# Optimization experiments

Measured on AMD Instinct MI355X. Metric: run time of the kernel, lower is better.

## Reference

```python
import jax, jax.numpy as jnp
import numpy as np

ALPHA_FAST = 0.74
ALPHA_SLOW = 0.95
EPS = 1e-6


def setup_inputs() -> dict:
    key = jax.random.key(0)
    kA, kU = jax.random.split(key)
    A = jax.random.normal(kA, (8, 16, 64, 64, 64), dtype=jnp.float32)      # [B,M,T,H,W]
    U = jax.random.normal(kU, (8, 16, 2, 64, 64, 64), dtype=jnp.float32)   # [B,M,2,T,H,W]
    return {"A": A, "U": U}


def _ema_last(x, alpha):
    # Closed form of the causal EMA recurrence acc_t = a*acc_{t-1} + (1-a)*x_t,
    # evaluated only at the final timestep (the torch module discards all others):
    # acc_{T-1} = (1-a) * sum_t a^{T-1-t} x_t
    T = x.shape[2]
    t = jnp.arange(T)
    w = ((1.0 - alpha) * alpha ** (T - 1 - t)).astype(x.dtype)
    return jnp.einsum('bmthw,t->bmhw', x, w)


def _quad_energy_last(p):
    # p: [B,M,T,H,W]. quad_energy shifts by 2 frames (edge-replicated); at the
    # last frame: pq = 0.5*(p[T-1] - p[T-3])  (T >= 3).
    pq = 0.5 * (p[:, :, -1] - p[:, :, -3])
    return jnp.sqrt(jnp.maximum(p[:, :, -1] ** 2 + pq ** 2, EPS))


def reference(A, U):
    A_last = A[:, :, -1]                         # [B,M,H,W]
    A_fast = _ema_last(A, ALPHA_FAST)
    A_slow = _ema_last(A, ALPHA_SLOW)
    # torch.diff with prepend -> last element is A[T-1] - A[T-2]
    A_deriv = A[:, :, -1] - A[:, :, -2]
    E_re = _quad_energy_last(U[:, :, 0])
    E_im = _quad_energy_last(U[:, :, 1])
    E_temp = jnp.sqrt(jnp.maximum(E_re ** 2 + E_im ** 2, EPS))
    return jnp.concatenate([A_last, A_fast, A_slow, A_deriv, E_temp], axis=1)  # [B,5M,H,W]
```

## Files before the change

### kernel.cpp

```cpp
#include <hip/hip_runtime.h>
#include <math.h>


#define T_DIM 64
#define HW    4096
#define HALF_T 32

typedef __attribute__((ext_vector_type(4))) float f4v;

__device__ __forceinline__ f4v ntload4(const float* p) {
    return __builtin_nontemporal_load((const f4v*)p);
}

__global__ __launch_bounds__(256, 4) void temporal_summarizer_kernel(
        const float* __restrict__ A, const float* __restrict__ U,
        float* __restrict__ out, float pf32, float ps32) {
    constexpr float AF = 0.74f, AS = 0.95f;
    constexpr float OMF = 1.0f - 0.74f, OMS = 1.0f - 0.95f;
    constexpr float EPS = 1e-6f;

    const int blk   = blockIdx.x;
    const int hh    = blk & 1;
    const int split = (blk >> 1) & 3;
    const int bm    = blk >> 3;
    const int m     = bm & 15;
    const int b     = bm >> 4;

    const int pix = split * (HW / 4) + threadIdx.x * 4;

    const float* pA = A + (size_t)bm * (T_DIM * HW) + (size_t)(hh * HALF_T) * HW + pix;

    f4v fast = 0.f, slow = 0.f;
    f4v a62 = 0.f, a63 = 0.f;

    #pragma unroll 16
    for (int t = 0; t < HALF_T; ++t) {
        f4v x = ntload4(pA + (size_t)t * HW);
        fast = AF * fast + OMF * x;
        slow = AS * slow + OMS * x;
        if (hh && t == HALF_T - 2) a62 = x;
        if (hh && t == HALF_T - 1) a63 = x;
    }

    if (!hh) {
        fast *= pf32;
        slow *= ps32;
    }

    float* ofast = out + ((size_t)(b * 80 + 16 + m)) * HW + pix;
    float* oslow = out + ((size_t)(b * 80 + 32 + m)) * HW + pix;
    #pragma unroll
    for (int i = 0; i < 4; ++i) {
        atomicAdd(&ofast[i], fast[i]);
        atomicAdd(&oslow[i], slow[i]);
    }

    if (hh) {
        const float* pU = U + (size_t)bm * (2 * T_DIM * HW) + pix;
        f4v u0l = ntload4(pU + 63 * HW);
        f4v u0m = ntload4(pU + 61 * HW);
        f4v u1l = ntload4(pU + (size_t)T_DIM * HW + 63 * HW);
        f4v u1m = ntload4(pU + (size_t)T_DIM * HW + 61 * HW);

        f4v et;
        #pragma unroll
        for (int i = 0; i < 4; ++i) {
            float pq0 = 0.5f * (u0l[i] - u0m[i]);
            float er  = sqrtf(fmaxf(u0l[i] * u0l[i] + pq0 * pq0, EPS));
            float pq1 = 0.5f * (u1l[i] - u1m[i]);
            float ei  = sqrtf(fmaxf(u1l[i] * u1l[i] + pq1 * pq1, EPS));
            et[i] = sqrtf(fmaxf(er * er + ei * ei, EPS));
        }

        f4v deriv = a63 - a62;

        float* ob = out + ((size_t)(b * 80 + m)) * HW + pix;
        *(f4v*)(ob + 0 * 16 * HW) = a63;
        *(f4v*)(ob + 48 * HW)     = deriv;
        *(f4v*)(ob + 64 * HW)     = et;
    }
}

extern "C" void kernel_launch(void* const* d_in, const int* in_sizes, int n_in,
                              void* d_out, int out_size, void* d_ws, size_t ws_size,
                              hipStream_t stream) {
    const float* A = (const float*)d_in[0];
    const float* U = (const float*)d_in[1];
    float* out = (float*)d_out;

    hipMemsetAsync(out, 0, (size_t)out_size * sizeof(float), stream);

    const float pf32 = (float)pow(0.74, 32.0);
    const float ps32 = (float)pow(0.95, 32.0);

    dim3 grid(8 * 16 * 4 * 2);
    dim3 block(256);
    temporal_summarizer_kernel<<<grid, block, 0, stream>>>(A, U, out, pf32, ps32);
}
```

Baseline: 390.2 us.

## Drop temporal split and atomics; one block per pixel tile over full T

Removes the two-way split of the time axis, so each block walks all 64 frames and writes every output with plain nontemporal stores. This eliminates the memset launch and the float atomicAdds on the fast and slow EMA outputs. The cost is half the grid (512 blocks) with longer, fully unrolled serial chains per thread, so there is less parallelism to hide memory latency. The et loop is computed twice, and the second loop overwrites the first, which wastes a few instructions.

Result: faster. 366.2 us (-6.2%).

```diff
diff --git a/kernel.cpp b/kernel.cpp
--- a/kernel.cpp
+++ b/kernel.cpp
@@ -4,81 +4,77 @@
 
 #define T_DIM 64
 #define HW    4096
-#define HALF_T 32
 
 typedef __attribute__((ext_vector_type(4))) float f4v;
 
 __device__ __forceinline__ f4v ntload4(const float* p) {
     return __builtin_nontemporal_load((const f4v*)p);
 }
+__device__ __forceinline__ void ntstore4(float* p, f4v v) {
+    __builtin_nontemporal_store(v, (f4v*)p);
+}
 
-__global__ __launch_bounds__(256, 4) void temporal_summarizer_kernel(
+__global__ __launch_bounds__(256) void temporal_summarizer_kernel(
         const float* __restrict__ A, const float* __restrict__ U,
-        float* __restrict__ out, float pf32, float ps32) {
+        float* __restrict__ out) {
     constexpr float AF = 0.74f, AS = 0.95f;
     constexpr float OMF = 1.0f - 0.74f, OMS = 1.0f - 0.95f;
     constexpr float EPS = 1e-6f;
 
     const int blk   = blockIdx.x;
-    const int hh    = blk & 1;
-    const int split = (blk >> 1) & 3;
-    const int bm    = blk >> 3;
+    const int split = blk & 3;
+    const int bm    = blk >> 2;
     const int m     = bm & 15;
     const int b     = bm >> 4;
 
     const int pix = split * (HW / 4) + threadIdx.x * 4;
 
-    const float* pA = A + (size_t)bm * (T_DIM * HW) + (size_t)(hh * HALF_T) * HW + pix;
+    const float* pA = A + (size_t)bm * (T_DIM * HW) + pix;
 
     f4v fast = 0.f, slow = 0.f;
     f4v a62 = 0.f, a63 = 0.f;
 
-    #pragma unroll 16
-    for (int t = 0; t < HALF_T; ++t) {
+    #pragma unroll
+    for (int t = 0; t < T_DIM; ++t) {
         f4v x = ntload4(pA + (size_t)t * HW);
         fast = AF * fast + OMF * x;
         slow = AS * slow + OMS * x;
-        if (hh && t == HALF_T - 2) a62 = x;
-        if (hh && t == HALF_T - 1) a63 = x;
+        if (t == T_DIM - 2) a62 = x;
+        if (t == T_DIM - 1) a63 = x;
     }
 
-    if (!hh) {
-        fast *= pf32;
-        slow *= ps32;
+    const float* pU = U + (size_t)bm * (2 * T_DIM * HW) + pix;
+    f4v u0l = ntload4(pU + 63 * HW);
+    f4v u0m = ntload4(pU + 61 * HW);
+    f4v u1l = ntload4(pU + (size_t)T_DIM * HW + 63 * HW);
+    f4v u1m = ntload4(pU + (size_t)T_DIM * HW + 61 * HW);
+
+    f4v et;
+    #pragma unroll
+    for (int i = 0; i < 4; ++i) {
+        float pq0 = 0.5f * (u0l[i] - u0m[i]);
+        float er2 = fmaxf(u0l[i] * u0l[i] + pq0 * pq0, EPS);
+        float pq1 = 0.5f * (u1l[i] - u1m[i]);
+        float ei2 = fmaxf(u1l[i] * u1l[i] + pq1 * pq1, EPS);
+        et[i] = sqrtf(fmaxf(er2 + ei2, EPS));
+    }
+    #pragma unroll
+    for (int i = 0; i < 4; ++i) {
+        float pq0 = 0.5f * (u0l[i] - u0m[i]);
+        float er  = sqrtf(fmaxf(u0l[i] * u0l[i] + pq0 * pq0, EPS));
+        float pq1 = 0.5f * (u1l[i] - u1m[i]);
+        float ei  = sqrtf(fmaxf(u1l[i] * u1l[i] + pq1 * pq1, EPS));
+        et[i] = sqrtf(fmaxf(er * er + ei * ei, EPS));
     }
 
-    float* ofast = out + ((size_t)(b * 80 + 16 + m)) * HW + pix;
-    float* oslow = out + ((size_t)(b * 80 + 32 + m)) * HW + pix;
-    #pragma unroll
-    for (int i = 0; i < 4; ++i) {
-        atomicAdd(&ofast[i], fast[i]);
-        atomicAdd(&oslow[i], slow[i]);
-    }
+    f4v deriv = a63 - a62;
 
-    if (hh) {
-        const float* pU = U + (size_t)bm * (2 * T_DIM * HW) + pix;
-        f4v u0l = ntload4(pU + 63 * HW);
-        f4v u0m = ntload4(pU + 61 * HW);
-        f4v u1l = ntload4(pU + (size_t)T_DIM * HW + 63 * HW);
-        f4v u1m = ntload4(pU + (size_t)T_DIM * HW + 61 * HW);
-
-        f4v et;
-        #pragma unroll
-        for (int i = 0; i < 4; ++i) {
-            float pq0 = 0.5f * (u0l[i] - u0m[i]);
-            float er  = sqrtf(fmaxf(u0l[i] * u0l[i] + pq0 * pq0, EPS));
-            float pq1 = 0.5f * (u1l[i] - u1m[i]);
-            float ei  = sqrtf(fmaxf(u1l[i] * u1l[i] + pq1 * pq1, EPS));
-            et[i] = sqrtf(fmaxf(er * er + ei * ei, EPS));
-        }
-
-        f4v deriv = a63 - a62;
-
-        float* ob = out + ((size_t)(b * 80 + m)) * HW + pix;
-        *(f4v*)(ob + 0 * 16 * HW) = a63;
-        *(f4v*)(ob + 48 * HW)     = deriv;
-        *(f4v*)(ob + 64 * HW)     = et;
-    }
+    float* ob = out + ((size_t)(b * 80 + m)) * HW + pix;
+    ntstore4(ob + 0 * 16 * HW, a63);
+    ntstore4(ob + 1 * 16 * HW, fast);
+    ntstore4(ob + 2 * 16 * HW, slow);
+    ntstore4(ob + 3 * 16 * HW, deriv);
+    ntstore4(ob + 4 * 16 * HW, et);
 }
 
 extern "C" void kernel_launch(void* const* d_in, const int* in_sizes, int n_in,
@@ -87,13 +83,7 @@
     const float* A = (const float*)d_in[0];
     const float* U = (const float*)d_in[1];
     float* out = (float*)d_out;
-
-    hipMemsetAsync(out, 0, (size_t)out_size * sizeof(float), stream);
-
-    const float pf32 = (float)pow(0.74, 32.0);
-    const float ps32 = (float)pow(0.95, 32.0);
-
-    dim3 grid(8 * 16 * 4 * 2);
+    dim3 grid(8 * 16 * 4);
     dim3 block(256);
-    temporal_summarizer_kernel<<<grid, block, 0, stream>>>(A, U, out, pf32, ps32);
+    temporal_summarizer_kernel<<<grid, block, 0, stream>>>(A, U, out);
 }
```
